# Optimization experiments

Hardware: AMD Instinct MI355X
Metric: run time of the kernel (lower is better)

Reference implementation:

```python
import jax, jax.numpy as jnp
import numpy as np

B, L, D = 8, 2048, 1024   # batch, seq_len, d_model
E, H, K = 8, 512, 2       # num_experts, expert_hidden, top_k
LN_EPS = 1e-5


def setup_inputs() -> dict:
    key = jax.random.key(0)
    ks = jax.random.split(key, 4)
    rn = lambda k, shape, sc: (jax.random.normal(k, shape, jnp.float32) * sc)
    return {
        "x": rn(ks[0], (B, L, D), 1.0),
        "ln_w": jnp.ones((D,), jnp.float32),
        "ln_b": jnp.zeros((D,), jnp.float32),
        "gate_w": rn(ks[1], (D, E), 0.02),
        "gate_b": jnp.zeros((E,), jnp.float32),
        "w1": rn(ks[2], (E, D, H), 0.02),
        "b1": jnp.zeros((E, H), jnp.float32),
        "w2": rn(ks[3], (E, H, D), 0.02),
        "b2": jnp.zeros((E, D), jnp.float32),
    }


def reference(x, ln_w, ln_b, gate_w, gate_b, w1, b1, w2, b2):
    Bx, Lx, Dx = x.shape
    xf = x.reshape(-1, Dx)                                   # [N, D]

    # gate = LayerNorm -> Linear (eval mode: no noise)
    mu = xf.mean(-1, keepdims=True)
    var = ((xf - mu) ** 2).mean(-1, keepdims=True)
    xn = (xf - mu) * jax.lax.rsqrt(var + LN_EPS) * ln_w + ln_b
    gate_logits = xn @ gate_w + gate_b                       # [N, E]
    gate_weights = jax.nn.softmax(gate_logits, axis=-1)      # [N, E]

    top_w, top_idx = jax.lax.top_k(gate_weights, K)          # [N, K]
    top_w = top_w / top_w.sum(-1, keepdims=True)

    # dense all-experts compute (faithful to the torch module)
    h = jax.nn.gelu(jnp.einsum('nd,edh->neh', xf, w1) + b1, approximate=False)  # [N, E, H]
    expert_out = jnp.einsum('neh,ehd->ned', h, w2) + b2      # [N, E, D]

    # gather selected experts and weighted-combine
    sel = jnp.take_along_axis(expert_out, top_idx[:, :, None], axis=1)  # [N, K, D]
    out = (top_w[:, :, None] * sel).sum(axis=1).reshape(Bx, Lx, Dx)
    return out, gate_weights
```

## Files before the change

kernel.cpp:

```cpp
#include <hip/hip_runtime.h>
#include <hip/hip_bf16.h>

#define N_TOK 16384
#define DM 1024
#define HD 512
#define NE 8
#define LN_EPS 1e-5f
#define MT_MAX 264

typedef __attribute__((ext_vector_type(8))) short v8s;
typedef __attribute__((ext_vector_type(4))) float v4f;

typedef const __attribute__((address_space(1))) unsigned int* as1cu;
typedef __attribute__((address_space(3))) unsigned int* as3u;

__device__ __forceinline__ void gl_lds16(const void* g, void* l) {
  __builtin_amdgcn_global_load_lds((as1cu)g, (as3u)l, 16, 0, 0);
}

__device__ __forceinline__ unsigned short f2bf(float f) {
  union { float f; unsigned u; } c; c.f = f;
  unsigned u = c.u + 0x7FFFu + ((c.u >> 16) & 1u);
  return (unsigned short)(u >> 16);
}

__device__ __forceinline__ float gelu_f(float v) {
  return 0.5f * v * (1.0f + erff(v * 0.7071067811865475f));
}

__global__ __launch_bounds__(256) void gate_kernel(
    const float* __restrict__ x, const float* __restrict__ lnw,
    const float* __restrict__ lnb, const float* __restrict__ gw,
    const float* __restrict__ gb, float* __restrict__ gates_out,
    int* __restrict__ ce, float* __restrict__ cw,
    unsigned short* __restrict__ xbf)
{
  const int wv = threadIdx.x >> 6, l = threadIdx.x & 63;
  const int n = blockIdx.x * 4 + wv;
  const float* xr = x + (size_t)n * DM;
  float4 v[4]; float s = 0.f, s2 = 0.f;
#pragma unroll
  for (int j = 0; j < 4; ++j) {
    v[j] = *(const float4*)(xr + l * 4 + j * 256);
    s  += v[j].x + v[j].y + v[j].z + v[j].w;
    s2 += v[j].x * v[j].x + v[j].y * v[j].y + v[j].z * v[j].z + v[j].w * v[j].w;
  }
  if (xbf) {
    unsigned long long* xbo = (unsigned long long*)(xbf + (size_t)n * DM);
#pragma unroll
    for (int j = 0; j < 4; ++j) {
      union { unsigned short u[4]; unsigned long long ll; } pk;
      pk.u[0] = f2bf(v[j].x); pk.u[1] = f2bf(v[j].y);
      pk.u[2] = f2bf(v[j].z); pk.u[3] = f2bf(v[j].w);
      xbo[l + j * 64] = pk.ll;
    }
  }
#pragma unroll
  for (int m = 1; m < 64; m <<= 1) { s += __shfl_xor(s, m); s2 += __shfl_xor(s2, m); }
  const float mu = s * (1.f / DM);
  const float var = s2 * (1.f / DM) - mu * mu;
  const float rstd = 1.f / sqrtf(var + LN_EPS);
  float acc[8] = {0, 0, 0, 0, 0, 0, 0, 0};
#pragma unroll
  for (int j = 0; j < 4; ++j) {
#pragma unroll
    for (int q = 0; q < 4; ++q) {
      int d = l * 4 + j * 256 + q;
      float xv = (q == 0) ? v[j].x : (q == 1) ? v[j].y : (q == 2) ? v[j].z : v[j].w;
      float xn = (xv - mu) * rstd * lnw[d] + lnb[d];
      const float4 g0 = *(const float4*)(gw + d * 8);
      const float4 g1 = *(const float4*)(gw + d * 8 + 4);
      acc[0] += xn * g0.x; acc[1] += xn * g0.y; acc[2] += xn * g0.z; acc[3] += xn * g0.w;
      acc[4] += xn * g1.x; acc[5] += xn * g1.y; acc[6] += xn * g1.z; acc[7] += xn * g1.w;
    }
  }
#pragma unroll
  for (int e = 0; e < 8; ++e)
#pragma unroll
    for (int m = 1; m < 64; m <<= 1) acc[e] += __shfl_xor(acc[e], m);

  if (l == 0) {
    float lg[8], p[8], g[8];
    float mx = -1e30f;
    for (int e = 0; e < 8; ++e) { lg[e] = acc[e] + gb[e]; mx = fmaxf(mx, lg[e]); }
    float sum = 0.f;
    for (int e = 0; e < 8; ++e) { p[e] = expf(lg[e] - mx); sum += p[e]; }
    float inv = 1.f / sum;
    for (int e = 0; e < 8; ++e) g[e] = p[e] * inv;
    float4* go = (float4*)(gates_out + (size_t)n * 8);
    go[0] = make_float4(g[0], g[1], g[2], g[3]);
    go[1] = make_float4(g[4], g[5], g[6], g[7]);
    int e0 = 0; float b0 = g[0];
    for (int e = 1; e < 8; ++e) if (g[e] > b0) { b0 = g[e]; e0 = e; }
    int e1 = -1; float b1v = -1.f;
    for (int e = 0; e < 8; ++e) if (e != e0 && g[e] > b1v) { b1v = g[e]; e1 = e; }
    float wsum = b0 + b1v;
    ce[2 * n] = e0; ce[2 * n + 1] = e1;
    cw[2 * n] = b0 / wsum; cw[2 * n + 1] = b1v / wsum;
  }
}

__global__ __launch_bounds__(256) void route_kernel(
    const int* __restrict__ ce, const float* __restrict__ cw,
    int* __restrict__ counts, int* __restrict__ tids, float* __restrict__ pws)
{
  __shared__ int cnt;
  const int e = blockIdx.x;
  if (threadIdx.x == 0) cnt = 0;
  __syncthreads();
  for (int i = threadIdx.x; i < 2 * N_TOK; i += 256) {
    if (ce[i] == e) {
      int p = atomicAdd(&cnt, 1);
      tids[e * N_TOK + p] = i >> 1;
      pws[e * N_TOK + p] = cw[i];
    }
  }
  __syncthreads();
  if (threadIdx.x == 0) counts[e] = cnt;
}

__global__ __launch_bounds__(256) void transpose_cvt(
    const float* __restrict__ in, unsigned short* __restrict__ out, int R, int C)
{
  __shared__ float tile[64][65];
  const int tilesC = C >> 6, tilesR = R >> 6;
  const int perE = tilesR * tilesC;
  int bt = blockIdx.x;
  const int e = bt / perE; int rem = bt - e * perE;
  const int tr = rem / tilesC, tc = rem - tr * tilesC;
  const float* ip = in + (size_t)e * R * C;
  unsigned short* op = out + (size_t)e * R * C;
  const int r0 = tr * 64, c0 = tc * 64;
#pragma unroll
  for (int i = 0; i < 16; ++i) {
    int idx = i * 256 + threadIdx.x;
    int rr = idx >> 6, cc = idx & 63;
    tile[rr][cc] = ip[(size_t)(r0 + rr) * C + (c0 + cc)];
  }
  __syncthreads();
#pragma unroll
  for (int i = 0; i < 16; ++i) {
    int idx = i * 256 + threadIdx.x;
    int rr = idx >> 6, cc = idx & 63;
    op[(size_t)(c0 + rr) * R + (r0 + cc)] = f2bf(tile[cc][rr]);
  }
}

__global__ __launch_bounds__(256, 3) void gemm1_kernel(
    const unsigned short* __restrict__ xbf, const unsigned short* __restrict__ w1t,
    const float* __restrict__ b1,
    const int* __restrict__ counts, const int* __restrict__ tids,
    unsigned short* __restrict__ hbuf)
{
  __shared__ unsigned short As[128 * 64];
  __shared__ unsigned short Bs[128 * 64];
  __shared__ int tokL[128];
  __shared__ int sE, sBase, sCnt;

  const int t = threadIdx.x;
  const int bid = blockIdx.x;
  const int nt = bid / MT_MAX;
  const int mt = bid - nt * MT_MAX;

  if (t == 0) {
    int pref = 0, e = -1, base = 0, cn = 0;
    for (int i = 0; i < NE; ++i) {
      int c = counts[i];
      int tiles = (c + 127) >> 7;
      if (mt < pref + tiles) { e = i; base = (mt - pref) << 7; cn = c; break; }
      pref += tiles;
    }
    sE = e; sBase = base; sCnt = cn;
  }
  __syncthreads();
  const int e = sE;
  if (e < 0) return;
  const int cnt = sCnt, baseI = sBase;

  if (t < 128) {
    int i = baseI + t;
    tokL[t] = (i < cnt) ? tids[e * N_TOK + i] : tids[e * N_TOK];
  }
  __syncthreads();

  const unsigned short* gA[4];
  const unsigned short* gB[4];
#pragma unroll
  for (int i = 0; i < 4; ++i) {
    int c = i * 256 + t;
    int row = c >> 3, ks = c & 7;
    int kswz = ks ^ (row & 7);
    gA[i] = xbf + (size_t)tokL[row] * DM + kswz * 8;
    gB[i] = w1t + ((size_t)e * HD + nt * 128 + row) * DM + kswz * 8;
  }
  const int w = t >> 6, l = t & 63;
  const int wr = w >> 1, wc = w & 1;
  const int lrow = l & 15, lhi = l >> 4;
  char* AsB = (char*)As;
  char* BsB = (char*)Bs;
  char* ldsA = AsB + w * 1024;
  char* ldsB = BsB + w * 1024;

  v4f acc[4][4];
#pragma unroll
  for (int a = 0; a < 4; ++a)
#pragma unroll
    for (int b = 0; b < 4; ++b) acc[a][b] = (v4f){0.f, 0.f, 0.f, 0.f};

  for (int kt = 0; kt < 16; ++kt) {
    __syncthreads();
#pragma unroll
    for (int i = 0; i < 4; ++i) {
      gl_lds16(gA[i] + kt * 64, ldsA + i * 4096);
      gl_lds16(gB[i] + kt * 64, ldsB + i * 4096);
    }
    __syncthreads();
#pragma unroll
    for (int ks2 = 0; ks2 < 2; ++ks2) {
      const int sb = ks2 * 4 + lhi;
      v8s a[4], b[4];
#pragma unroll
      for (int mi = 0; mi < 4; ++mi) {
        int row = wr * 64 + mi * 16 + lrow;
        a[mi] = *(const v8s*)(AsB + row * 128 + ((sb ^ (row & 7)) << 4));
      }
#pragma unroll
      for (int nj = 0; nj < 4; ++nj) {
        int col = wc * 64 + nj * 16 + lrow;
        b[nj] = *(const v8s*)(BsB + col * 128 + ((sb ^ (col & 7)) << 4));
      }
#pragma unroll
      for (int mi = 0; mi < 4; ++mi)
#pragma unroll
        for (int nj = 0; nj < 4; ++nj)
          acc[mi][nj] = __builtin_amdgcn_mfma_f32_16x16x32_bf16(a[mi], b[nj], acc[mi][nj], 0, 0, 0);
    }
  }

#pragma unroll
  for (int nj = 0; nj < 4; ++nj) {
    const int col = nt * 128 + wc * 64 + nj * 16 + lrow;
    const float bb = b1[e * HD + col];
#pragma unroll
    for (int mi = 0; mi < 4; ++mi) {
      const int row0 = wr * 64 + mi * 16 + lhi * 4;
#pragma unroll
      for (int r = 0; r < 4; ++r) {
        float g = gelu_f(acc[mi][nj][r] + bb);
        hbuf[(size_t)(mt * 128 + row0 + r) * HD + col] = f2bf(g);
      }
    }
  }
}

__global__ __launch_bounds__(256, 3) void gemm2_kernel(
    const unsigned short* __restrict__ hbuf, const unsigned short* __restrict__ w2t,
    const float* __restrict__ b2,
    const int* __restrict__ counts, const int* __restrict__ tids,
    const float* __restrict__ pws, float* __restrict__ outp)
{
  __shared__ unsigned short As[128 * 64];
  __shared__ unsigned short Bs[128 * 64];
  __shared__ int tokL[128];
  __shared__ float wtL[128];
  __shared__ int sE, sBase, sCnt;

  const int t = threadIdx.x;
  const int bid = blockIdx.x;
  const int nt = bid / MT_MAX;
  const int mt = bid - nt * MT_MAX;

  if (t == 0) {
    int pref = 0, e = -1, base = 0, cn = 0;
    for (int i = 0; i < NE; ++i) {
      int c = counts[i];
      int tiles = (c + 127) >> 7;
      if (mt < pref + tiles) { e = i; base = (mt - pref) << 7; cn = c; break; }
      pref += tiles;
    }
    sE = e; sBase = base; sCnt = cn;
  }
  __syncthreads();
  const int e = sE;
  if (e < 0) return;
  const int cnt = sCnt, baseI = sBase;

  if (t < 128) {
    int i = baseI + t;
    bool ok = i < cnt;
    tokL[t] = ok ? tids[e * N_TOK + i] : 0;
    wtL[t] = ok ? pws[e * N_TOK + i] : 0.f;
  }
  __syncthreads();

  const unsigned short* gA[4];
  const unsigned short* gB[4];
#pragma unroll
  for (int i = 0; i < 4; ++i) {
    int c = i * 256 + t;
    int row = c >> 3, ks = c & 7;
    int kswz = ks ^ (row & 7);
    gA[i] = hbuf + (size_t)(mt * 128 + row) * HD + kswz * 8;
    gB[i] = w2t + ((size_t)e * DM + nt * 128 + row) * HD + kswz * 8;
  }
  const int w = t >> 6, l = t & 63;
  const int wr = w >> 1, wc = w & 1;
  const int lrow = l & 15, lhi = l >> 4;
  char* AsB = (char*)As;
  char* BsB = (char*)Bs;
  char* ldsA = AsB + w * 1024;
  char* ldsB = BsB + w * 1024;

  v4f acc[4][4];
#pragma unroll
  for (int a = 0; a < 4; ++a)
#pragma unroll
    for (int b = 0; b < 4; ++b) acc[a][b] = (v4f){0.f, 0.f, 0.f, 0.f};

  for (int kt = 0; kt < 8; ++kt) {
    __syncthreads();
#pragma unroll
    for (int i = 0; i < 4; ++i) {
      gl_lds16(gA[i] + kt * 64, ldsA + i * 4096);
      gl_lds16(gB[i] + kt * 64, ldsB + i * 4096);
    }
    __syncthreads();
#pragma unroll
    for (int ks2 = 0; ks2 < 2; ++ks2) {
      const int sb = ks2 * 4 + lhi;
      v8s a[4], b[4];
#pragma unroll
      for (int mi = 0; mi < 4; ++mi) {
        int row = wr * 64 + mi * 16 + lrow;
        a[mi] = *(const v8s*)(AsB + row * 128 + ((sb ^ (row & 7)) << 4));
      }
#pragma unroll
      for (int nj = 0; nj < 4; ++nj) {
        int col = wc * 64 + nj * 16 + lrow;
        b[nj] = *(const v8s*)(BsB + col * 128 + ((sb ^ (col & 7)) << 4));
      }
#pragma unroll
      for (int mi = 0; mi < 4; ++mi)
#pragma unroll
        for (int nj = 0; nj < 4; ++nj)
          acc[mi][nj] = __builtin_amdgcn_mfma_f32_16x16x32_bf16(a[mi], b[nj], acc[mi][nj], 0, 0, 0);
    }
  }

#pragma unroll
  for (int nj = 0; nj < 4; ++nj) {
    const int col = nt * 128 + wc * 64 + nj * 16 + lrow;
    const float bb = b2[e * DM + col];
#pragma unroll
    for (int mi = 0; mi < 4; ++mi) {
      const int rbase = wr * 64 + mi * 16 + lhi * 4;
#pragma unroll
      for (int r = 0; r < 4; ++r) {
        const int rloc = rbase + r;
        if (baseI + rloc < cnt) {
          float val = wtL[rloc] * (acc[mi][nj][r] + bb);
          atomicAdd(outp + (size_t)tokL[rloc] * DM + col, val);
        }
      }
    }
  }
}

#define H_OFF   0
#define XS_OFF  65536
#define W1S_OFF 73728
#define W2S_OFF 65536
#define TOK_OFF 139264
#define WT_OFF  139520
#define SMEM_BYTES 139776

template<bool FULL>
__global__ __launch_bounds__(512, 2) void ffn_kernel(
    const float* __restrict__ x,
    const float* __restrict__ w1, const float* __restrict__ b1,
    const float* __restrict__ w2, const float* __restrict__ b2,
    const unsigned short* __restrict__ w1t, const unsigned short* __restrict__ w2t,
    const int* __restrict__ counts, const int* __restrict__ tids,
    const float* __restrict__ pws, float* __restrict__ outp)
{
  extern __shared__ char smem[];
  const int e = blockIdx.x & 7;
  const int tile = blockIdx.x >> 3;
  const int cnt = counts[e];
  const int base = tile * 64;
  if (base >= cnt) return;
  const int t = threadIdx.x;
  const int w = t >> 6, l = t & 63;
  const int lrow = l & 15, lhi = l >> 4;

  int* tokL = (int*)(smem + TOK_OFF);
  float* wtL = (float*)(smem + WT_OFF);
  if (t < 64) {
    int i = base + t;
    bool ok = i < cnt;
    int src = e * N_TOK + (ok ? i : base);
    tokL[t] = tids[src];
    wtL[t] = ok ? pws[src] : 0.f;
  }
  __syncthreads();

  v4f acc[4][4];
#pragma unroll
  for (int a = 0; a < 4; ++a)
#pragma unroll
    for (int b = 0; b < 4; ++b) acc[a][b] = (v4f){0.f, 0.f, 0.f, 0.f};

  for (int kt = 0; kt < 16; ++kt) {
    const int k0 = kt * 64;
    {
      const int tokr = t >> 3, ks = t & 7;
      const float* src = x + (size_t)tokL[tokr] * DM + k0 + ks * 8;
      float f[8];
      *(float4*)(f) = *(const float4*)src;
      *(float4*)(f + 4) = *(const float4*)(src + 4);
      v8s pv;
#pragma unroll
      for (int j = 0; j < 8; ++j) pv[j] = (short)f2bf(f[j]);
      *(v8s*)(smem + XS_OFF + tokr * 128 + ((ks ^ (tokr & 7)) << 4)) = pv;
    }
    if (FULL) {
#pragma unroll
      for (int i = 0; i < 8; ++i) {
        int c = i * 512 + t;
        int h = c >> 3, ks = c & 7;
        v8s val = *(const v8s*)(w1t + ((size_t)e * HD + h) * DM + k0 + ks * 8);
        *(v8s*)(smem + W1S_OFF + h * 128 + ((ks ^ (h & 7)) << 4)) = val;
      }
    } else {
      const int h = t;
#pragma unroll
      for (int i = 0; i < 8; ++i) {
        float f[8];
#pragma unroll
        for (int j = 0; j < 8; ++j) f[j] = w1[((size_t)e * DM + k0 + i * 8 + j) * HD + h];
        v8s pv;
#pragma unroll
        for (int j = 0; j < 8; ++j) pv[j] = (short)f2bf(f[j]);
        *(v8s*)(smem + W1S_OFF + h * 128 + ((i ^ (h & 7)) << 4)) = pv;
      }
    }
    __syncthreads();
#pragma unroll
    for (int ks2 = 0; ks2 < 2; ++ks2) {
      const int sb = (ks2 << 2) + lhi;
      v8s af[4], bfr[4];
#pragma unroll
      for (int mi = 0; mi < 4; ++mi) {
        int row = mi * 16 + lrow;
        af[mi] = *(const v8s*)(smem + XS_OFF + row * 128 + ((sb ^ (row & 7)) << 4));
      }
#pragma unroll
      for (int nj = 0; nj < 4; ++nj) {
        int col = (w << 6) + nj * 16 + lrow;
        bfr[nj] = *(const v8s*)(smem + W1S_OFF + col * 128 + ((sb ^ (col & 7)) << 4));
      }
#pragma unroll
      for (int mi = 0; mi < 4; ++mi)
#pragma unroll
        for (int nj = 0; nj < 4; ++nj)
          acc[mi][nj] = __builtin_amdgcn_mfma_f32_16x16x32_bf16(af[mi], bfr[nj], acc[mi][nj], 0, 0, 0);
    }
    __syncthreads();
  }

#pragma unroll
  for (int nj = 0; nj < 4; ++nj) {
    const int col = (w << 6) + nj * 16 + lrow;
    const float b1v = b1[e * HD + col];
#pragma unroll
    for (int mi = 0; mi < 4; ++mi) {
#pragma unroll
      for (int r = 0; r < 4; ++r) {
        int row = mi * 16 + lhi * 4 + r;
        float g = gelu_f(acc[mi][nj][r] + b1v);
        *(unsigned short*)(smem + H_OFF + row * 1024 + ((col * 2) ^ ((row & 7) << 4))) = f2bf(g);
      }
    }
  }
  __syncthreads();

  for (int nc = 0; nc < 4; ++nc) {
    v4f acc2[4][2];
#pragma unroll
    for (int a = 0; a < 4; ++a)
#pragma unroll
      for (int b = 0; b < 2; ++b) acc2[a][b] = (v4f){0.f, 0.f, 0.f, 0.f};
    for (int k2 = 0; k2 < 8; ++k2) {
      const int h0 = k2 * 64;
      if (FULL) {
#pragma unroll
        for (int i = 0; i < 4; ++i) {
          int c = i * 512 + t;
          int dloc = c >> 3, ks = c & 7;
          v8s val = *(const v8s*)(w2t + ((size_t)e * DM + nc * 256 + dloc) * HD + h0 + ks * 8);
          *(v8s*)(smem + W2S_OFF + dloc * 128 + ((ks ^ (dloc & 7)) << 4)) = val;
        }
      } else {
        const int dloc = t & 255;
        const int kb = t >> 8;
#pragma unroll
        for (int i = 0; i < 4; ++i) {
          int ks = kb + i * 2;
          float f[8];
#pragma unroll
          for (int j = 0; j < 8; ++j) f[j] = w2[((size_t)e * HD + h0 + ks * 8 + j) * DM + nc * 256 + dloc];
          v8s pv;
#pragma unroll
          for (int j = 0; j < 8; ++j) pv[j] = (short)f2bf(f[j]);
          *(v8s*)(smem + W2S_OFF + dloc * 128 + ((ks ^ (dloc & 7)) << 4)) = pv;
        }
      }
      __syncthreads();
#pragma unroll
      for (int ks2 = 0; ks2 < 2; ++ks2) {
        const int sb = (ks2 << 2) + lhi;
        v8s af[4], bfr[2];
#pragma unroll
        for (int mi = 0; mi < 4; ++mi) {
          int row = mi * 16 + lrow;
          int slin = (h0 >> 3) + sb;
          af[mi] = *(const v8s*)(smem + H_OFF + row * 1024 + ((slin ^ (row & 7)) << 4));
        }
#pragma unroll
        for (int nj = 0; nj < 2; ++nj) {
          int dl = (w << 5) + nj * 16 + lrow;
          bfr[nj] = *(const v8s*)(smem + W2S_OFF + dl * 128 + ((sb ^ (dl & 7)) << 4));
        }
#pragma unroll
        for (int mi = 0; mi < 4; ++mi)
#pragma unroll
          for (int nj = 0; nj < 2; ++nj)
            acc2[mi][nj] = __builtin_amdgcn_mfma_f32_16x16x32_bf16(af[mi], bfr[nj], acc2[mi][nj], 0, 0, 0);
      }
      __syncthreads();
    }
#pragma unroll
    for (int nj = 0; nj < 2; ++nj) {
      const int dl = (w << 5) + nj * 16 + lrow;
      const int d = nc * 256 + dl;
      const float b2v = b2[e * DM + d];
#pragma unroll
      for (int mi = 0; mi < 4; ++mi) {
#pragma unroll
        for (int r = 0; r < 4; ++r) {
          int row = mi * 16 + lhi * 4 + r;
          float val = wtL[row] * (acc2[mi][nj][r] + b2v);
          atomicAdd(outp + (size_t)tokL[row] * DM + d, val);
        }
      }
    }
  }
}

extern "C" void kernel_launch(void* const* d_in, const int* in_sizes, int n_in,
                              void* d_out, int out_size, void* d_ws, size_t ws_size,
                              hipStream_t stream)
{
  const float* x   = (const float*)d_in[0];
  const float* lnw = (const float*)d_in[1];
  const float* lnb = (const float*)d_in[2];
  const float* gw  = (const float*)d_in[3];
  const float* gb  = (const float*)d_in[4];
  const float* w1  = (const float*)d_in[5];
  const float* b1  = (const float*)d_in[6];
  const float* w2  = (const float*)d_in[7];
  const float* b2  = (const float*)d_in[8];
  float* out = (float*)d_out;
  float* gates_out = out + (size_t)N_TOK * DM;

  char* ws = (char*)d_ws;
  int*   ce     = (int*)(ws + 0);
  float* cw     = (float*)(ws + 131072);
  int*   counts = (int*)(ws + 262144);
  int*   tids   = (int*)(ws + 262400);
  float* pws    = (float*)(ws + 786688);
  unsigned short* w1t = (unsigned short*)(ws + 1310976);
  unsigned short* w2t = (unsigned short*)(ws + 9699584);
  unsigned short* xbf = (unsigned short*)(ws + 18088192);
  unsigned short* hbuf = (unsigned short*)(ws + 51642624);
  const size_t NEED_NEW = 86245632ull;
  const size_t NEED_FULL = 18088192ull;

  hipMemsetAsync(d_out, 0, (size_t)N_TOK * DM * sizeof(float), stream);

  if (ws_size >= NEED_NEW) {
    gate_kernel<<<N_TOK / 4, 256, 0, stream>>>(x, lnw, lnb, gw, gb, gates_out, ce, cw, xbf);
    route_kernel<<<NE, 256, 0, stream>>>(ce, cw, counts, tids, pws);
    transpose_cvt<<<NE * 16 * 8, 256, 0, stream>>>(w1, w1t, DM, HD);
    transpose_cvt<<<NE * 8 * 16, 256, 0, stream>>>(w2, w2t, HD, DM);
    gemm1_kernel<<<4 * MT_MAX, 256, 0, stream>>>(xbf, w1t, b1, counts, tids, hbuf);
    gemm2_kernel<<<8 * MT_MAX, 256, 0, stream>>>(hbuf, w2t, b2, counts, tids, pws, out);
  } else {
    gate_kernel<<<N_TOK / 4, 256, 0, stream>>>(x, lnw, lnb, gw, gb, gates_out, ce, cw, nullptr);
    route_kernel<<<NE, 256, 0, stream>>>(ce, cw, counts, tids, pws);
    if (ws_size >= NEED_FULL) {
      transpose_cvt<<<NE * 16 * 8, 256, 0, stream>>>(w1, w1t, DM, HD);
      transpose_cvt<<<NE * 8 * 16, 256, 0, stream>>>(w2, w2t, HD, DM);
      hipFuncSetAttribute((const void*)&ffn_kernel<true>,
                          hipFuncAttributeMaxDynamicSharedMemorySize, SMEM_BYTES);
      ffn_kernel<true><<<NE * 256, 512, SMEM_BYTES, stream>>>(
          x, w1, b1, w2, b2, w1t, w2t, counts, tids, pws, out);
    } else {
      hipFuncSetAttribute((const void*)&ffn_kernel<false>,
                          hipFuncAttributeMaxDynamicSharedMemorySize, SMEM_BYTES);
      ffn_kernel<false><<<NE * 256, 512, SMEM_BYTES, stream>>>(
          x, w1, b1, w2, b2, w1t, w2t, counts, tids, pws, out);
    }
  }
}
```

Baseline: 506.8 us.

## Widen GEMM N-tiles to 256 and replace atomic scatter with bf16 slot buffer plus combine

```diff
diff --git a/kernel.cpp b/kernel.cpp
--- a/kernel.cpp
+++ b/kernel.cpp
@@ -24,6 +24,11 @@
   return (unsigned short)(u >> 16);
 }
 
+__device__ __forceinline__ float bf2f(unsigned short v) {
+  union { unsigned u; float f; } c; c.u = ((unsigned)v) << 16;
+  return c.f;
+}
+
 __device__ __forceinline__ float gelu_f(float v) {
   return 0.5f * v * (1.0f + erff(v * 0.7071067811865475f));
 }
@@ -45,7 +50,7 @@
     s  += v[j].x + v[j].y + v[j].z + v[j].w;
     s2 += v[j].x * v[j].x + v[j].y * v[j].y + v[j].z * v[j].z + v[j].w * v[j].w;
   }
-  if (xbf) {
+  {
     unsigned long long* xbo = (unsigned long long*)(xbf + (size_t)n * DM);
 #pragma unroll
     for (int j = 0; j < 4; ++j) {
@@ -111,7 +116,7 @@
   for (int i = threadIdx.x; i < 2 * N_TOK; i += 256) {
     if (ce[i] == e) {
       int p = atomicAdd(&cnt, 1);
-      tids[e * N_TOK + p] = i >> 1;
+      tids[e * N_TOK + p] = i;
       pws[e * N_TOK + p] = cw[i];
     }
   }
@@ -146,14 +151,14 @@
   }
 }
 
-__global__ __launch_bounds__(256, 3) void gemm1_kernel(
+__global__ __launch_bounds__(256) void gemm1w_kernel(
     const unsigned short* __restrict__ xbf, const unsigned short* __restrict__ w1t,
     const float* __restrict__ b1,
     const int* __restrict__ counts, const int* __restrict__ tids,
     unsigned short* __restrict__ hbuf)
 {
   __shared__ unsigned short As[128 * 64];
-  __shared__ unsigned short Bs[128 * 64];
+  __shared__ unsigned short Bs[256 * 64];
   __shared__ int tokL[128];
   __shared__ int sE, sBase, sCnt;
 
@@ -179,19 +184,21 @@
 
   if (t < 128) {
     int i = baseI + t;
-    tokL[t] = (i < cnt) ? tids[e * N_TOK + i] : tids[e * N_TOK];
+    tokL[t] = ((i < cnt) ? tids[e * N_TOK + i] : tids[e * N_TOK]) >> 1;
   }
   __syncthreads();
 
   const unsigned short* gA[4];
-  const unsigned short* gB[4];
 #pragma unroll
   for (int i = 0; i < 4; ++i) {
     int c = i * 256 + t;
     int row = c >> 3, ks = c & 7;
-    int kswz = ks ^ (row & 7);
-    gA[i] = xbf + (size_t)tokL[row] * DM + kswz * 8;
-    gB[i] = w1t + ((size_t)e * HD + nt * 128 + row) * DM + kswz * 8;
+    gA[i] = xbf + (size_t)tokL[row] * DM + (ks ^ (row & 7)) * 8;
+  }
+  const unsigned short* gB0;
+  {
+    int row = t >> 3, ks = t & 7;
+    gB0 = w1t + ((size_t)e * HD + nt * 256 + row) * DM + (ks ^ (row & 7)) * 8;
   }
   const int w = t >> 6, l = t & 63;
   const int wr = w >> 1, wc = w & 1;
@@ -201,45 +208,46 @@
   char* ldsA = AsB + w * 1024;
   char* ldsB = BsB + w * 1024;
 
-  v4f acc[4][4];
+  v4f acc[4][8];
 #pragma unroll
   for (int a = 0; a < 4; ++a)
 #pragma unroll
-    for (int b = 0; b < 4; ++b) acc[a][b] = (v4f){0.f, 0.f, 0.f, 0.f};
+    for (int b = 0; b < 8; ++b) acc[a][b] = (v4f){0.f, 0.f, 0.f, 0.f};
 
   for (int kt = 0; kt < 16; ++kt) {
     __syncthreads();
 #pragma unroll
-    for (int i = 0; i < 4; ++i) {
+    for (int i = 0; i < 4; ++i)
       gl_lds16(gA[i] + kt * 64, ldsA + i * 4096);
-      gl_lds16(gB[i] + kt * 64, ldsB + i * 4096);
-    }
+#pragma unroll
+    for (int i = 0; i < 8; ++i)
+      gl_lds16(gB0 + (size_t)i * 32 * DM + kt * 64, ldsB + i * 4096);
     __syncthreads();
 #pragma unroll
     for (int ks2 = 0; ks2 < 2; ++ks2) {
       const int sb = ks2 * 4 + lhi;
-      v8s a[4], b[4];
+      v8s a[4], b[8];
 #pragma unroll
       for (int mi = 0; mi < 4; ++mi) {
         int row = wr * 64 + mi * 16 + lrow;
         a[mi] = *(const v8s*)(AsB + row * 128 + ((sb ^ (row & 7)) << 4));
       }
 #pragma unroll
-      for (int nj = 0; nj < 4; ++nj) {
-        int col = wc * 64 + nj * 16 + lrow;
+      for (int nj = 0; nj < 8; ++nj) {
+        int col = wc * 128 + nj * 16 + lrow;
         b[nj] = *(const v8s*)(BsB + col * 128 + ((sb ^ (col & 7)) << 4));
       }
 #pragma unroll
       for (int mi = 0; mi < 4; ++mi)
 #pragma unroll
-        for (int nj = 0; nj < 4; ++nj)
+        for (int nj = 0; nj < 8; ++nj)
           acc[mi][nj] = __builtin_amdgcn_mfma_f32_16x16x32_bf16(a[mi], b[nj], acc[mi][nj], 0, 0, 0);
     }
   }
 
 #pragma unroll
-  for (int nj = 0; nj < 4; ++nj) {
-    const int col = nt * 128 + wc * 64 + nj * 16 + lrow;
+  for (int nj = 0; nj < 8; ++nj) {
+    const int col = nt * 256 + wc * 128 + nj * 16 + lrow;
     const float bb = b1[e * HD + col];
 #pragma unroll
     for (int mi = 0; mi < 4; ++mi) {
@@ -253,15 +261,15 @@
   }
 }
 
-__global__ __launch_bounds__(256, 3) void gemm2_kernel(
+__global__ __launch_bounds__(256) void gemm2w_kernel(
     const unsigned short* __restrict__ hbuf, const unsigned short* __restrict__ w2t,
     const float* __restrict__ b2,
     const int* __restrict__ counts, const int* __restrict__ tids,
-    const float* __restrict__ pws, float* __restrict__ outp)
+    const float* __restrict__ pws, unsigned short* __restrict__ obuf)
 {
   __shared__ unsigned short As[128 * 64];
-  __shared__ unsigned short Bs[128 * 64];
-  __shared__ int tokL[128];
+  __shared__ unsigned short Bs[256 * 64];
+  __shared__ int pidL[128];
   __shared__ float wtL[128];
   __shared__ int sE, sBase, sCnt;
 
@@ -288,20 +296,18 @@
   if (t < 128) {
     int i = baseI + t;
     bool ok = i < cnt;
-    tokL[t] = ok ? tids[e * N_TOK + i] : 0;
+    pidL[t] = ok ? tids[e * N_TOK + i] : 0;
     wtL[t] = ok ? pws[e * N_TOK + i] : 0.f;
   }
   __syncthreads();
 
-  const unsigned short* gA[4];
-  const unsigned short* gB[4];
-#pragma unroll
-  for (int i = 0; i < 4; ++i) {
-    int c = i * 256 + t;
-    int row = c >> 3, ks = c & 7;
-    int kswz = ks ^ (row & 7);
-    gA[i] = hbuf + (size_t)(mt * 128 + row) * HD + kswz * 8;
-    gB[i] = w2t + ((size_t)e * DM + nt * 128 + row) * HD + kswz * 8;
+  const unsigned short* gA0;
+  const unsigned short* gB0;
+  {
+    int row = t >> 3, ks = t & 7;
+    int kswz = (ks ^ (row & 7)) * 8;
+    gA0 = hbuf + (size_t)(mt * 128 + row) * HD + kswz;
+    gB0 = w2t + ((size_t)e * DM + nt * 256 + row) * HD + kswz;
   }
   const int w = t >> 6, l = t & 63;
   const int wr = w >> 1, wc = w & 1;
@@ -311,6 +317,138 @@
   char* ldsA = AsB + w * 1024;
   char* ldsB = BsB + w * 1024;
 
+  v4f acc[4][8];
+#pragma unroll
+  for (int a = 0; a < 4; ++a)
+#pragma unroll
+    for (int b = 0; b < 8; ++b) acc[a][b] = (v4f){0.f, 0.f, 0.f, 0.f};
+
+  for (int kt = 0; kt < 8; ++kt) {
+    __syncthreads();
+#pragma unroll
+    for (int i = 0; i < 4; ++i)
+      gl_lds16(gA0 + (size_t)i * 32 * HD + kt * 64, ldsA + i * 4096);
+#pragma unroll
+    for (int i = 0; i < 8; ++i)
+      gl_lds16(gB0 + (size_t)i * 32 * HD + kt * 64, ldsB + i * 4096);
+    __syncthreads();
+#pragma unroll
+    for (int ks2 = 0; ks2 < 2; ++ks2) {
+      const int sb = ks2 * 4 + lhi;
+      v8s a[4], b[8];
+#pragma unroll
+      for (int mi = 0; mi < 4; ++mi) {
+        int row = wr * 64 + mi * 16 + lrow;
+        a[mi] = *(const v8s*)(AsB + row * 128 + ((sb ^ (row & 7)) << 4));
+      }
+#pragma unroll
+      for (int nj = 0; nj < 8; ++nj) {
+        int col = wc * 128 + nj * 16 + lrow;
+        b[nj] = *(const v8s*)(BsB + col * 128 + ((sb ^ (col & 7)) << 4));
+      }
+#pragma unroll
+      for (int mi = 0; mi < 4; ++mi)
+#pragma unroll
+        for (int nj = 0; nj < 8; ++nj)
+          acc[mi][nj] = __builtin_amdgcn_mfma_f32_16x16x32_bf16(a[mi], b[nj], acc[mi][nj], 0, 0, 0);
+    }
+  }
+
+#pragma unroll
+  for (int nj = 0; nj < 8; ++nj) {
+    const int col = nt * 256 + wc * 128 + nj * 16 + lrow;
+    const float bb = b2[e * DM + col];
+#pragma unroll
+    for (int mi = 0; mi < 4; ++mi) {
+      const int rbase = wr * 64 + mi * 16 + lhi * 4;
+#pragma unroll
+      for (int r = 0; r < 4; ++r) {
+        const int rloc = rbase + r;
+        if (baseI + rloc < cnt) {
+          float val = wtL[rloc] * (acc[mi][nj][r] + bb);
+          obuf[(size_t)pidL[rloc] * DM + col] = f2bf(val);
+        }
+      }
+    }
+  }
+}
+
+__global__ __launch_bounds__(256) void combine_kernel(
+    const unsigned short* __restrict__ obuf, float* __restrict__ outp)
+{
+  const int CH = N_TOK * (DM / 8);
+  for (int i = blockIdx.x * 256 + threadIdx.x; i < CH; i += gridDim.x * 256) {
+    const int n = i >> 7, rem = i & 127;
+    const v8s a = *(const v8s*)(obuf + ((size_t)(2 * n)) * DM + rem * 8);
+    const v8s b = *(const v8s*)(obuf + ((size_t)(2 * n + 1)) * DM + rem * 8);
+    float o[8];
+#pragma unroll
+    for (int j = 0; j < 8; ++j)
+      o[j] = bf2f((unsigned short)a[j]) + bf2f((unsigned short)b[j]);
+    float* dst = outp + (size_t)n * DM + rem * 8;
+    *(float4*)dst = make_float4(o[0], o[1], o[2], o[3]);
+    *(float4*)(dst + 4) = make_float4(o[4], o[5], o[6], o[7]);
+  }
+}
+
+__global__ __launch_bounds__(256, 3) void gemm2_kernel(
+    const unsigned short* __restrict__ hbuf, const unsigned short* __restrict__ w2t,
+    const float* __restrict__ b2,
+    const int* __restrict__ counts, const int* __restrict__ tids,
+    const float* __restrict__ pws, float* __restrict__ outp)
+{
+  __shared__ unsigned short As[128 * 64];
+  __shared__ unsigned short Bs[128 * 64];
+  __shared__ int tokL[128];
+  __shared__ float wtL[128];
+  __shared__ int sE, sBase, sCnt;
+
+  const int t = threadIdx.x;
+  const int bid = blockIdx.x;
+  const int nt = bid / MT_MAX;
+  const int mt = bid - nt * MT_MAX;
+
+  if (t == 0) {
+    int pref = 0, e = -1, base = 0, cn = 0;
+    for (int i = 0; i < NE; ++i) {
+      int c = counts[i];
+      int tiles = (c + 127) >> 7;
+      if (mt < pref + tiles) { e = i; base = (mt - pref) << 7; cn = c; break; }
+      pref += tiles;
+    }
+    sE = e; sBase = base; sCnt = cn;
+  }
+  __syncthreads();
+  const int e = sE;
+  if (e < 0) return;
+  const int cnt = sCnt, baseI = sBase;
+
+  if (t < 128) {
+    int i = baseI + t;
+    bool ok = i < cnt;
+    tokL[t] = ok ? (tids[e * N_TOK + i] >> 1) : 0;
+    wtL[t] = ok ? pws[e * N_TOK + i] : 0.f;
+  }
+  __syncthreads();
+
+  const unsigned short* gA[4];
+  const unsigned short* gB[4];
+#pragma unroll
+  for (int i = 0; i < 4; ++i) {
+    int c = i * 256 + t;
+    int row = c >> 3, ks = c & 7;
+    int kswz = ks ^ (row & 7);
+    gA[i] = hbuf + (size_t)(mt * 128 + row) * HD + kswz * 8;
+    gB[i] = w2t + ((size_t)e * DM + nt * 128 + row) * HD + kswz * 8;
+  }
+  const int w = t >> 6, l = t & 63;
+  const int wr = w >> 1, wc = w & 1;
+  const int lrow = l & 15, lhi = l >> 4;
+  char* AsB = (char*)As;
+  char* BsB = (char*)Bs;
+  char* ldsA = AsB + w * 1024;
+  char* ldsB = BsB + w * 1024;
+
   v4f acc[4][4];
 #pragma unroll
   for (int a = 0; a < 4; ++a)
@@ -360,197 +498,6 @@
         if (baseI + rloc < cnt) {
           float val = wtL[rloc] * (acc[mi][nj][r] + bb);
           atomicAdd(outp + (size_t)tokL[rloc] * DM + col, val);
-        }
-      }
-    }
-  }
-}
-
-#define H_OFF   0
-#define XS_OFF  65536
-#define W1S_OFF 73728
-#define W2S_OFF 65536
-#define TOK_OFF 139264
-#define WT_OFF  139520
-#define SMEM_BYTES 139776
-
-template<bool FULL>
-__global__ __launch_bounds__(512, 2) void ffn_kernel(
-    const float* __restrict__ x,
-    const float* __restrict__ w1, const float* __restrict__ b1,
-    const float* __restrict__ w2, const float* __restrict__ b2,
-    const unsigned short* __restrict__ w1t, const unsigned short* __restrict__ w2t,
-    const int* __restrict__ counts, const int* __restrict__ tids,
-    const float* __restrict__ pws, float* __restrict__ outp)
-{
-  extern __shared__ char smem[];
-  const int e = blockIdx.x & 7;
-  const int tile = blockIdx.x >> 3;
-  const int cnt = counts[e];
-  const int base = tile * 64;
-  if (base >= cnt) return;
-  const int t = threadIdx.x;
-  const int w = t >> 6, l = t & 63;
-  const int lrow = l & 15, lhi = l >> 4;
-
-  int* tokL = (int*)(smem + TOK_OFF);
-  float* wtL = (float*)(smem + WT_OFF);
-  if (t < 64) {
-    int i = base + t;
-    bool ok = i < cnt;
-    int src = e * N_TOK + (ok ? i : base);
-    tokL[t] = tids[src];
-    wtL[t] = ok ? pws[src] : 0.f;
-  }
-  __syncthreads();
-
-  v4f acc[4][4];
-#pragma unroll
-  for (int a = 0; a < 4; ++a)
-#pragma unroll
-    for (int b = 0; b < 4; ++b) acc[a][b] = (v4f){0.f, 0.f, 0.f, 0.f};
-
-  for (int kt = 0; kt < 16; ++kt) {
-    const int k0 = kt * 64;
-    {
-      const int tokr = t >> 3, ks = t & 7;
-      const float* src = x + (size_t)tokL[tokr] * DM + k0 + ks * 8;
-      float f[8];
-      *(float4*)(f) = *(const float4*)src;
-      *(float4*)(f + 4) = *(const float4*)(src + 4);
-      v8s pv;
-#pragma unroll
-      for (int j = 0; j < 8; ++j) pv[j] = (short)f2bf(f[j]);
-      *(v8s*)(smem + XS_OFF + tokr * 128 + ((ks ^ (tokr & 7)) << 4)) = pv;
-    }
-    if (FULL) {
-#pragma unroll
-      for (int i = 0; i < 8; ++i) {
-        int c = i * 512 + t;
-        int h = c >> 3, ks = c & 7;
-        v8s val = *(const v8s*)(w1t + ((size_t)e * HD + h) * DM + k0 + ks * 8);
-        *(v8s*)(smem + W1S_OFF + h * 128 + ((ks ^ (h & 7)) << 4)) = val;
-      }
-    } else {
-      const int h = t;
-#pragma unroll
-      for (int i = 0; i < 8; ++i) {
-        float f[8];
-#pragma unroll
-        for (int j = 0; j < 8; ++j) f[j] = w1[((size_t)e * DM + k0 + i * 8 + j) * HD + h];
-        v8s pv;
-#pragma unroll
-        for (int j = 0; j < 8; ++j) pv[j] = (short)f2bf(f[j]);
-        *(v8s*)(smem + W1S_OFF + h * 128 + ((i ^ (h & 7)) << 4)) = pv;
-      }
-    }
-    __syncthreads();
-#pragma unroll
-    for (int ks2 = 0; ks2 < 2; ++ks2) {
-      const int sb = (ks2 << 2) + lhi;
-      v8s af[4], bfr[4];
-#pragma unroll
-      for (int mi = 0; mi < 4; ++mi) {
-        int row = mi * 16 + lrow;
-        af[mi] = *(const v8s*)(smem + XS_OFF + row * 128 + ((sb ^ (row & 7)) << 4));
-      }
-#pragma unroll
-      for (int nj = 0; nj < 4; ++nj) {
-        int col = (w << 6) + nj * 16 + lrow;
-        bfr[nj] = *(const v8s*)(smem + W1S_OFF + col * 128 + ((sb ^ (col & 7)) << 4));
-      }
-#pragma unroll
-      for (int mi = 0; mi < 4; ++mi)
-#pragma unroll
-        for (int nj = 0; nj < 4; ++nj)
-          acc[mi][nj] = __builtin_amdgcn_mfma_f32_16x16x32_bf16(af[mi], bfr[nj], acc[mi][nj], 0, 0, 0);
-    }
-    __syncthreads();
-  }
-
-#pragma unroll
-  for (int nj = 0; nj < 4; ++nj) {
-    const int col = (w << 6) + nj * 16 + lrow;
-    const float b1v = b1[e * HD + col];
-#pragma unroll
-    for (int mi = 0; mi < 4; ++mi) {
-#pragma unroll
-      for (int r = 0; r < 4; ++r) {
-        int row = mi * 16 + lhi * 4 + r;
-        float g = gelu_f(acc[mi][nj][r] + b1v);
-        *(unsigned short*)(smem + H_OFF + row * 1024 + ((col * 2) ^ ((row & 7) << 4))) = f2bf(g);
-      }
-    }
-  }
-  __syncthreads();
-
-  for (int nc = 0; nc < 4; ++nc) {
-    v4f acc2[4][2];
-#pragma unroll
-    for (int a = 0; a < 4; ++a)
-#pragma unroll
-      for (int b = 0; b < 2; ++b) acc2[a][b] = (v4f){0.f, 0.f, 0.f, 0.f};
-    for (int k2 = 0; k2 < 8; ++k2) {
-      const int h0 = k2 * 64;
-      if (FULL) {
-#pragma unroll
-        for (int i = 0; i < 4; ++i) {
-          int c = i * 512 + t;
-          int dloc = c >> 3, ks = c & 7;
-          v8s val = *(const v8s*)(w2t + ((size_t)e * DM + nc * 256 + dloc) * HD + h0 + ks * 8);
-          *(v8s*)(smem + W2S_OFF + dloc * 128 + ((ks ^ (dloc & 7)) << 4)) = val;
-        }
-      } else {
-        const int dloc = t & 255;
-        const int kb = t >> 8;
-#pragma unroll
-        for (int i = 0; i < 4; ++i) {
-          int ks = kb + i * 2;
-          float f[8];
-#pragma unroll
-          for (int j = 0; j < 8; ++j) f[j] = w2[((size_t)e * HD + h0 + ks * 8 + j) * DM + nc * 256 + dloc];
-          v8s pv;
-#pragma unroll
-          for (int j = 0; j < 8; ++j) pv[j] = (short)f2bf(f[j]);
-          *(v8s*)(smem + W2S_OFF + dloc * 128 + ((ks ^ (dloc & 7)) << 4)) = pv;
-        }
-      }
-      __syncthreads();
-#pragma unroll
-      for (int ks2 = 0; ks2 < 2; ++ks2) {
-        const int sb = (ks2 << 2) + lhi;
-        v8s af[4], bfr[2];
-#pragma unroll
-        for (int mi = 0; mi < 4; ++mi) {
-          int row = mi * 16 + lrow;
-          int slin = (h0 >> 3) + sb;
-          af[mi] = *(const v8s*)(smem + H_OFF + row * 1024 + ((slin ^ (row & 7)) << 4));
-        }
-#pragma unroll
-        for (int nj = 0; nj < 2; ++nj) {
-          int dl = (w << 5) + nj * 16 + lrow;
-          bfr[nj] = *(const v8s*)(smem + W2S_OFF + dl * 128 + ((sb ^ (dl & 7)) << 4));
-        }
-#pragma unroll
-        for (int mi = 0; mi < 4; ++mi)
-#pragma unroll
-          for (int nj = 0; nj < 2; ++nj)
-            acc2[mi][nj] = __builtin_amdgcn_mfma_f32_16x16x32_bf16(af[mi], bfr[nj], acc2[mi][nj], 0, 0, 0);
-      }
-      __syncthreads();
-    }
-#pragma unroll
-    for (int nj = 0; nj < 2; ++nj) {
-      const int dl = (w << 5) + nj * 16 + lrow;
-      const int d = nc * 256 + dl;
-      const float b2v = b2[e * DM + d];
-#pragma unroll
-      for (int mi = 0; mi < 4; ++mi) {
-#pragma unroll
-        for (int r = 0; r < 4; ++r) {
-          int row = mi * 16 + lhi * 4 + r;
-          float val = wtL[row] * (acc2[mi][nj][r] + b2v);
-          atomicAdd(outp + (size_t)tokL[row] * DM + d, val);
         }
       }
     }
@@ -579,37 +526,24 @@
   int*   counts = (int*)(ws + 262144);
   int*   tids   = (int*)(ws + 262400);
   float* pws    = (float*)(ws + 786688);
-  unsigned short* w1t = (unsigned short*)(ws + 1310976);
-  unsigned short* w2t = (unsigned short*)(ws + 9699584);
-  unsigned short* xbf = (unsigned short*)(ws + 18088192);
+  unsigned short* w1t  = (unsigned short*)(ws + 1310976);
+  unsigned short* w2t  = (unsigned short*)(ws + 9699584);
+  unsigned short* xbf  = (unsigned short*)(ws + 18088192);
   unsigned short* hbuf = (unsigned short*)(ws + 51642624);
-  const size_t NEED_NEW = 86245632ull;
-  const size_t NEED_FULL = 18088192ull;
-
-  hipMemsetAsync(d_out, 0, (size_t)N_TOK * DM * sizeof(float), stream);
-
-  if (ws_size >= NEED_NEW) {
-    gate_kernel<<<N_TOK / 4, 256, 0, stream>>>(x, lnw, lnb, gw, gb, gates_out, ce, cw, xbf);
-    route_kernel<<<NE, 256, 0, stream>>>(ce, cw, counts, tids, pws);
-    transpose_cvt<<<NE * 16 * 8, 256, 0, stream>>>(w1, w1t, DM, HD);
-    transpose_cvt<<<NE * 8 * 16, 256, 0, stream>>>(w2, w2t, HD, DM);
-    gemm1_kernel<<<4 * MT_MAX, 256, 0, stream>>>(xbf, w1t, b1, counts, tids, hbuf);
+  unsigned short* obuf = (unsigned short*)(ws + 86245632);
+  const size_t NEED_V3 = 153354496ull;
+
+  gate_kernel<<<N_TOK / 4, 256, 0, stream>>>(x, lnw, lnb, gw, gb, gates_out, ce, cw, xbf);
+  route_kernel<<<NE, 256, 0, stream>>>(ce, cw, counts, tids, pws);
+  transpose_cvt<<<NE * 16 * 8, 256, 0, stream>>>(w1, w1t, DM, HD);
+  transpose_cvt<<<NE * 8 * 16, 256, 0, stream>>>(w2, w2t, HD, DM);
+  gemm1w_kernel<<<2 * MT_MAX, 256, 0, stream>>>(xbf, w1t, b1, counts, tids, hbuf);
+
+  if (ws_size >= NEED_V3) {
+    gemm2w_kernel<<<4 * MT_MAX, 256, 0, stream>>>(hbuf, w2t, b2, counts, tids, pws, obuf);
+    combine_kernel<<<2048, 256, 0, stream>>>(obuf, out);
+  } else {
+    hipMemsetAsync(out, 0, (size_t)N_TOK * DM * sizeof(float), stream);
     gemm2_kernel<<<8 * MT_MAX, 256, 0, stream>>>(hbuf, w2t, b2, counts, tids, pws, out);
-  } else {
-    gate_kernel<<<N_TOK / 4, 256, 0, stream>>>(x, lnw, lnb, gw, gb, gates_out, ce, cw, nullptr);
-    route_kernel<<<NE, 256, 0, stream>>>(ce, cw, counts, tids, pws);
-    if (ws_size >= NEED_FULL) {
-      transpose_cvt<<<NE * 16 * 8, 256, 0, stream>>>(w1, w1t, DM, HD);
-      transpose_cvt<<<NE * 8 * 16, 256, 0, stream>>>(w2, w2t, HD, DM);
-      hipFuncSetAttribute((const void*)&ffn_kernel<true>,
-                          hipFuncAttributeMaxDynamicSharedMemorySize, SMEM_BYTES);
-      ffn_kernel<true><<<NE * 256, 512, SMEM_BYTES, stream>>>(
-          x, w1, b1, w2, b2, w1t, w2t, counts, tids, pws, out);
-    } else {
-      hipFuncSetAttribute((const void*)&ffn_kernel<false>,
-                          hipFuncAttributeMaxDynamicSharedMemorySize, SMEM_BYTES);
-      ffn_kernel<false><<<NE * 256, 512, SMEM_BYTES, stream>>>(
-          x, w1, b1, w2, b2, w1t, w2t, counts, tids, pws, out);
-    }
-  }
-}
+  }
+}
```

New measurement: 595.7 us. 1.18x slower.
